# Kernel optimization log

Measured on AMD Instinct MI355X. Metric: run time of the kernel, lower is better.

## Reference

```python
import jax, jax.numpy as jnp
import numpy as np

DIM = 512; NHEAD = 8; DHEAD = 64; INNER = NHEAD * DHEAD
CTX = 1024; NOCT = int(np.ceil(np.log2(CTX))) + 1  # 11
B = 8; SEQ = 256; MEM = 768


def positional_encoding(ctx, num_oct):
    # matches Attention.positional_encoding on coords=arange(ctx).view(ctx,1),
    # start_octave = 1 - num_oct
    coords = jnp.arange(ctx, dtype=jnp.float32)[:, None, None]        # (ctx,1,1)
    octaves = jnp.arange(1 - num_oct, 1, dtype=jnp.float32)           # (num_oct,)
    mult = (2.0 ** octaves) * np.pi
    scaled = (coords * mult).reshape(ctx, num_oct)                    # (ctx, num_oct)
    return jnp.concatenate([jnp.sin(scaled), jnp.cos(scaled)], axis=-1)  # (ctx, 2*num_oct)


def get_shifts(mem, seq, ctx):
    coords = jnp.arange(mem + seq - 1, -1, -1) - (seq - 1)            # (mem+seq,)
    shifts = coords[None, :] + jnp.arange(seq)[:, None]               # (seq, mem+seq)
    oob = (shifts < 0) | (shifts > ctx - 1)
    bias = jnp.where(oob, -jnp.inf, 0.0).astype(jnp.float32)
    return jnp.clip(shifts, 0, ctx - 1), bias


def setup_inputs() -> dict:
    key = jax.random.key(0)
    ks = jax.random.split(key, 8)
    s = 0.02
    return {
        "x": jax.random.normal(ks[0], (B, SEQ, DIM), jnp.float32),
        "memory": jax.random.normal(ks[1], (B, MEM, DIM), jnp.float32),
        "W_qkv": jax.random.normal(ks[2], (DIM, 3 * INNER), jnp.float32) * s,
        "W_rel": jax.random.normal(ks[3], (2 * NOCT, INNER), jnp.float32) * s,
        "W_out": jax.random.normal(ks[4], (INNER, DIM), jnp.float32) * s,
        "b_out": jnp.zeros((DIM,), jnp.float32),
        "u_emb": jax.random.normal(ks[5], (DHEAD,), jnp.float32),
        "v_emb": jax.random.normal(ks[6], (DHEAD,), jnp.float32),
    }


def reference(x, memory, W_qkv, W_rel, W_out, b_out, u_emb, v_emb):
    b, seq, _ = x.shape
    mem = memory.shape[1]
    total = mem + seq
    scale = DHEAD ** -0.5

    shifts, bias = get_shifts(mem, seq, CTX)                          # (seq,total) each
    R = positional_encoding(CTX, NOCT)                                # (CTX, 2*NOCT)
    kr = (R @ W_rel)[shifts].reshape(seq, total, NHEAD, DHEAD)        # n m h d

    qkv = jnp.concatenate([memory, x], axis=1) @ W_qkv                # (b,total,3*INNER)
    q, k, v = jnp.split(qkv, 3, axis=-1)

    def heads(t):
        return t.reshape(b, total, NHEAD, DHEAD).transpose(0, 2, 1, 3)  # b h m d

    q = heads(q)[:, :, mem:]                                          # b h n d (queries only over x)
    k = heads(k)
    v = heads(v)

    term_a = jnp.einsum('bhnd,bhmd->bhnm', q, k)
    term_b = jnp.einsum('bhnd,nmhd->bhnm', q, kr)
    term_c = jnp.einsum('d,bhmd->bhm', u_emb, k)[:, :, None, :]        # broadcast over n
    term_d = jnp.einsum('d,nmhd->hnm', v_emb, kr)[None]                # broadcast over b

    dots = (term_a + term_b + term_c + term_d) * scale + bias          # banded -inf mask
    attn = jax.nn.softmax(dots, axis=-1)                               # dropout p=0 -> identity
    out = jnp.einsum('bhnm,bhmd->bnhd', attn, v).reshape(b, seq, INNER)
    return out @ W_out + b_out
```

## Files before the change

### kernel.cpp

```cpp
#include <hip/hip_runtime.h>
#include <hip/hip_bf16.h>
#include <math.h>

typedef unsigned short u16;
typedef unsigned int u32;
typedef __attribute__((ext_vector_type(8))) short short8;
typedef __attribute__((ext_vector_type(4))) float floatx4;

constexpr int kB     = 8;
constexpr int kSEQ   = 256;
constexpr int kMEM   = 768;
constexpr int kTOTAL = 1024;

__device__ __forceinline__ float bf2f(u16 u) {
  return __uint_as_float(((u32)u) << 16);
}
__device__ __forceinline__ u16 f2bf(float f) {
  __hip_bfloat16 h = __float2bfloat16(f);
  return *reinterpret_cast<u16*>(&h);
}
__device__ __forceinline__ void gload_lds16(const u16* g, u16* l) {
  __builtin_amdgcn_global_load_lds(
      (__attribute__((address_space(1))) const unsigned int*)g,
      (__attribute__((address_space(3))) unsigned int*)l, 16, 0, 0);
}

__global__ __launch_bounds__(256) void rrel_kernel(
    const float* __restrict__ W_rel, const float* __restrict__ v_emb,
    u16* __restrict__ Rrel_bf, float* __restrict__ vR)
{
  __shared__ float pe[22];
  __shared__ float prod[512];
  int s = blockIdx.x;
  int t = threadIdx.x;
  if (t < 22) {
    int o = (t < 11) ? t : (t - 11);
    float mult = ldexpf(3.14159265358979323846f, o - 10);
    float ang = (float)s * mult;
    pe[t] = (t < 11) ? sinf(ang) : cosf(ang);
  }
  __syncthreads();
#pragma unroll
  for (int c = 0; c < 2; c++) {
    int j = t + c * 256;
    float acc = 0.f;
#pragma unroll
    for (int o = 0; o < 22; ++o) acc += pe[o] * W_rel[o * 512 + j];
    Rrel_bf[(size_t)s * 512 + j] = f2bf(acc);
    prod[j] = acc * v_emb[j & 63];
  }
  __syncthreads();
  if (t < 8) {
    float a = 0.f;
#pragma unroll 8
    for (int d = 0; d < 64; d++) a += prod[t * 64 + d];
    vR[t * 1024 + s] = a * 0.125f;
  }
}

__device__ __forceinline__ void wtconv_body(
    const float* __restrict__ W, u16* __restrict__ Wt, int K, int N,
    int n0, int k0, int tid, float (*tile)[65])
{
  int r = tid >> 4, c4 = (tid & 15) * 4;
#pragma unroll
  for (int v = 0; v < 4; v++) {
    float4 w4 = *(const float4*)(W + (size_t)(k0 + v * 16 + r) * N + n0 + c4);
    tile[v * 16 + r][c4 + 0] = w4.x;
    tile[v * 16 + r][c4 + 1] = w4.y;
    tile[v * 16 + r][c4 + 2] = w4.z;
    tile[v * 16 + r][c4 + 3] = w4.w;
  }
  __syncthreads();
#pragma unroll
  for (int v = 0; v < 4; v++) {
    int rn = v * 16 + r;
    ushort4 o;
    o.x = f2bf(tile[c4 + 0][rn]);
    o.y = f2bf(tile[c4 + 1][rn]);
    o.z = f2bf(tile[c4 + 2][rn]);
    o.w = f2bf(tile[c4 + 3][rn]);
    *(ushort4*)(Wt + (size_t)(n0 + rn) * K + k0 + c4) = o;
  }
}

__global__ __launch_bounds__(256) void xw_kernel(
    const float* __restrict__ x, const float* __restrict__ memf,
    const float* __restrict__ W_qkv, const float* __restrict__ W_out,
    u16* __restrict__ Xb, u16* __restrict__ WqkvT, u16* __restrict__ WoutT)
{
  __shared__ float tile[64][65];
  int bid = blockIdx.x;
  int tid = threadIdx.x;
  if (bid < 2048) {
    int idx = bid * 256 + tid;
    int row = idx >> 6, c8 = idx & 63;
    int b = row >> 10, pos = row & 1023;
    const float* src = (pos < kMEM)
        ? memf + (size_t)(b * kMEM + pos) * 512
        : x    + (size_t)(b * kSEQ + pos - kMEM) * 512;
    const float4* s4 = (const float4*)(src + c8 * 8);
    float4 a = s4[0], bb = s4[1];
    u16 tmp[8] = {f2bf(a.x),  f2bf(a.y),  f2bf(a.z),  f2bf(a.w),
                  f2bf(bb.x), f2bf(bb.y), f2bf(bb.z), f2bf(bb.w)};
    *(uint4*)(Xb + (size_t)row * 512 + c8 * 8) = *(uint4*)tmp;
  } else if (bid < 2240) {
    int r = bid - 2048;
    wtconv_body(W_qkv, WqkvT, 512, 1536, (r % 24) * 64, (r / 24) * 64, tid, tile);
  } else {
    int r = bid - 2240;
    wtconv_body(W_out, WoutT, 512, 512, (r % 8) * 64, (r / 8) * 64, tid, tile);
  }
}

__global__ __launch_bounds__(256) void gemm_bf16(
    const u16* __restrict__ A, const u16* __restrict__ Bt,
    int lda, int ldb, int ksteps,
    u16* __restrict__ Cbf, float* __restrict__ Cf, int ldc,
    const float* __restrict__ colAdd, int mode)
{
  __shared__ u16 As[128 * 64];
  __shared__ u16 Bs[128 * 64];
  int tid = threadIdx.x;
  int id = blockIdx.y * gridDim.x + blockIdx.x;
  int gy = gridDim.y;
  int bm = (id % gy) * 128, bn = (id / gy) * 128;
  int ln = tid & 15, quad = (tid >> 4) & 3, w = tid >> 6;
  int moff = (w >> 1) * 64, noff = (w & 1) * 64;
  int l7 = ln & 7;
  floatx4 acc[4][4];
#pragma unroll
  for (int mi = 0; mi < 4; mi++)
#pragma unroll
    for (int ni = 0; ni < 4; ni++) acc[mi][ni] = (floatx4){0.f, 0.f, 0.f, 0.f};

  int srow[4], sgch[4];
#pragma unroll
  for (int v = 0; v < 4; v++) {
    int f = v * 256 + tid;
    srow[v] = f >> 3;
    sgch[v] = (f & 7) ^ ((f >> 3) & 7);
  }

  for (int ks = 0; ks < ksteps; ks++) {
    int k0 = ks * 64;
#pragma unroll
    for (int v = 0; v < 4; v++) {
      gload_lds16(A + (size_t)(bm + srow[v]) * lda + k0 + sgch[v] * 8,
                  &As[(v * 256 + tid) * 8]);
      gload_lds16(Bt + (size_t)(bn + srow[v]) * ldb + k0 + sgch[v] * 8,
                  &Bs[(v * 256 + tid) * 8]);
    }
    __syncthreads();
#pragma unroll
    for (int kb = 0; kb < 2; kb++) {
      short8 af[4], bfr[4];
#pragma unroll
      for (int mi = 0; mi < 4; mi++) {
        int row = moff + mi * 16 + ln;
        af[mi] = *(const short8*)&As[row * 64 + (((quad + 4 * kb) ^ l7) << 3)];
      }
#pragma unroll
      for (int ni = 0; ni < 4; ni++) {
        int row = noff + ni * 16 + ln;
        bfr[ni] = *(const short8*)&Bs[row * 64 + (((quad + 4 * kb) ^ l7) << 3)];
      }
#pragma unroll
      for (int mi = 0; mi < 4; mi++)
#pragma unroll
        for (int ni = 0; ni < 4; ni++)
          acc[mi][ni] = __builtin_amdgcn_mfma_f32_16x16x32_bf16(
              af[mi], bfr[ni], acc[mi][ni], 0, 0, 0);
    }
    __syncthreads();
  }

  int r0 = bm + moff + quad * 4;
#pragma unroll
  for (int ni = 0; ni < 4; ni++) {
    int col = bn + noff + ni * 16 + ln;
    float cv = (mode == 2) ? colAdd[col] : 0.f;
    float scale = (mode == 0 && col < 512) ? 0.125f : 1.f;
#pragma unroll
    for (int mi = 0; mi < 4; mi++) {
#pragma unroll
      for (int r = 0; r < 4; r++) {
        int row = r0 + mi * 16 + r;
        float val = acc[mi][ni][r];
        if (mode == 2) Cf[(size_t)row * ldc + col] = val + cv;
        else           Cbf[(size_t)row * ldc + col] = f2bf(val * scale);
      }
    }
  }
}

__global__ __launch_bounds__(256) void uk_kernel(
    const u16* __restrict__ qkv_bf, const float* __restrict__ u_emb,
    float* __restrict__ uk)
{
  int idx = blockIdx.x * 256 + threadIdx.x;
  int b = idx >> 13, h = (idx >> 10) & 7, m = idx & 1023;
  const u16* kp = qkv_bf + (size_t)(b * kTOTAL + m) * 1536 + 512 + h * 64;
  const float4* ue4 = (const float4*)u_emb;
  float acc = 0.f;
#pragma unroll
  for (int c = 0; c < 8; c++) {
    uint4 raw = *(const uint4*)(kp + c * 8);
    const u16* us = (const u16*)&raw;
    float4 ua = ue4[2 * c], ub = ue4[2 * c + 1];
    acc += bf2f(us[0]) * ua.x + bf2f(us[1]) * ua.y + bf2f(us[2]) * ua.z + bf2f(us[3]) * ua.w
         + bf2f(us[4]) * ub.x + bf2f(us[5]) * ub.y + bf2f(us[6]) * ub.z + bf2f(us[7]) * ub.w;
  }
  uk[idx] = acc * 0.125f;
}

__global__ __launch_bounds__(256) void attn_mfma(
    const u16* __restrict__ qkv_bf, const u16* __restrict__ Rrel_bf,
    const float* __restrict__ vR, const float* __restrict__ uk,
    u16* __restrict__ Opart, float* __restrict__ lbuf)
{
  constexpr int LD  = 72;
  constexpr int TLD = 84;
  __shared__ u16 Vt[2][64 * LD];
  __shared__ u16 Ps[64 * LD];
  __shared__ u16 Tl[4 * 16 * TLD];

  int nt = blockIdx.x >> 3, p = blockIdx.x & 7;
  int h = blockIdx.y, b = blockIdx.z;
  int n0 = nt * 64, bh = b * 8 + h;
  int tid = threadIdx.x;
  int w = tid >> 6, lane = tid & 63;
  int l15 = lane & 15, quad = lane >> 4, q8 = quad * 8;

  int sr0 = tid >> 3, sc8 = tid & 7;
  int sr1 = (256 + tid) >> 3;
  int vg0 = ((sr0 >> 3) ^ sc8) * 8 + (sr0 & 7);
  int vg1 = ((sr1 >> 3) ^ sc8) * 8 + (sr1 & 7);

  const u16* qrow = qkv_bf + (size_t)(b * kTOTAL + kMEM + n0 + 16 * w + l15) * 1536 + h * 64;
  short8 qf0 = *(const short8*)(qrow + q8);
  short8 qf1 = *(const short8*)(qrow + 32 + q8);

  const u16* kpart = qkv_bf + (size_t)(b * kTOTAL) * 1536 + 512 + h * 64;
  const float* ukrow = uk + (size_t)bh * 1024 + l15;
  const float* vRh = vR + h * 1024;
  u16* Tw = Tl + w * 16 * TLD;

  int ntiles = 13 + nt;
  int mtA = p, mtB = p + 8;
  bool hasB = (mtB < ntiles);
  bool lastB = (mtB == ntiles - 1);

  {
    const u16* va = kpart + (size_t)mtA * 64 * 1536 + 512;
    const u16* vb = kpart + (size_t)mtB * 64 * 1536 + 512;
    uint4 a0 = *(const uint4*)(va + (size_t)sr0 * 1536 + sc8 * 8);
    uint4 a1 = *(const uint4*)(va + (size_t)sr1 * 1536 + sc8 * 8);
    uint4 b0 = *(const uint4*)(vb + (size_t)sr0 * 1536 + sc8 * 8);
    uint4 b1 = *(const uint4*)(vb + (size_t)sr1 * 1536 + sc8 * 8);
    const u16* pa0v = (const u16*)&a0;
    const u16* pa1v = (const u16*)&a1;
    const u16* pb0v = (const u16*)&b0;
    const u16* pb1v = (const u16*)&b1;
#pragma unroll
    for (int i = 0; i < 8; i++) {
      Vt[0][(sc8 * 8 + i) * LD + vg0] = pa0v[i];
      Vt[0][(sc8 * 8 + i) * LD + vg1] = pa1v[i];
      Vt[1][(sc8 * 8 + i) * LD + vg0] = pb0v[i];
      Vt[1][(sc8 * 8 + i) * LD + vg1] = pb1v[i];
    }
  }
  __syncthreads();

  floatx4 o_acc[4];
  float l_i[4];
#pragma unroll
  for (int r = 0; r < 4; r++) l_i[r] = 0.f;
#pragma unroll
  for (int nd = 0; nd < 4; nd++) o_acc[nd] = (floatx4){0.f, 0.f, 0.f, 0.f};

  int s_base_w = kMEM + n0 + 16 * w;

  auto tile_body = [&](int mt, bool lastt, const u16* VtX) {
    int m0 = mt * 64;
    const u16* kbase = kpart + (size_t)m0 * 1536;
    int sb = s_base_w - m0;

    short8 kb0[4], kb1[4];
#pragma unroll
    for (int ni = 0; ni < 4; ni++) {
      const u16* kr = kbase + (size_t)(16 * ni + l15) * 1536;
      kb0[ni] = *(const short8*)(kr + q8);
      kb1[ni] = *(const short8*)(kr + 32 + q8);
    }
    short8 rb0[5], rb1[5];
    float vRc[5];
#pragma unroll
    for (int ct = 0; ct < 5; ct++) {
      int s = sb - 63 + 16 * ct + l15;
      s = min(max(s, 0), 1023);
      const u16* rr = Rrel_bf + (size_t)s * 512 + h * 64;
      rb0[ct] = *(const short8*)(rr + q8);
      rb1[ct] = *(const short8*)(rr + 32 + q8);
      vRc[ct] = vRh[s];
    }
    float ukc[4];
#pragma unroll
    for (int ni = 0; ni < 4; ni++) ukc[ni] = ukrow[m0 + ni * 16];

#pragma unroll
    for (int ct = 0; ct < 5; ct++) {
      floatx4 t = (floatx4){0.f, 0.f, 0.f, 0.f};
      t = __builtin_amdgcn_mfma_f32_16x16x32_bf16(qf0, rb0[ct], t, 0, 0, 0);
      t = __builtin_amdgcn_mfma_f32_16x16x32_bf16(qf1, rb1[ct], t, 0, 0, 0);
#pragma unroll
      for (int r = 0; r < 4; r++)
        Tw[(4 * quad + r) * TLD + 16 * ct + l15] = f2bf(t[r] + vRc[ct]);
    }

    floatx4 s_acc[4];
#pragma unroll
    for (int ni = 0; ni < 4; ni++) {
      floatx4 sa = (floatx4){0.f, 0.f, 0.f, 0.f};
      sa = __builtin_amdgcn_mfma_f32_16x16x32_bf16(qf0, kb0[ni], sa, 0, 0, 0);
      sa = __builtin_amdgcn_mfma_f32_16x16x32_bf16(qf1, kb1[ni], sa, 0, 0, 0);
      s_acc[ni] = sa;
    }

#pragma unroll
    for (int r = 0; r < 4; r++) {
      int il = 4 * quad + r;
      float ls = 0.f;
      float pv[4];
#pragma unroll
      for (int ni = 0; ni < 4; ni++) {
        float tsh = bf2f(Tw[il * TLD + 63 + il - 16 * ni - l15]);
        float val = s_acc[ni][r] + tsh + ukc[ni];
        if (lastt && (16 * ni + l15) > (16 * w + il)) val = -1e30f;
        float e = __expf(val);
        pv[ni] = e;
        ls += e;
      }
      l_i[r] += ls;
      int prow = 16 * w + il;
      int rr3p = prow >> 3;
      int base = prow * LD + (l15 & 7);
#pragma unroll
      for (int ni = 0; ni < 4; ni++)
        Ps[base + (((2 * ni + (l15 >> 3)) ^ rr3p) << 3)] = f2bf(pv[ni]);
    }

    int rowq = 16 * w + l15, rr3q = rowq >> 3;
    short8 pa0 = *(const short8*)&Ps[rowq * LD + ((quad ^ rr3q) << 3)];
    short8 pa1 = *(const short8*)&Ps[rowq * LD + (((quad + 4) ^ rr3q) << 3)];
#pragma unroll
    for (int nd = 0; nd < 4; nd++) {
      int rowv = 16 * nd + l15, rr3v = rowv >> 3;
      short8 vb0 = *(const short8*)&VtX[rowv * LD + ((quad ^ rr3v) << 3)];
      short8 vb1 = *(const short8*)&VtX[rowv * LD + (((quad + 4) ^ rr3v) << 3)];
      o_acc[nd] = __builtin_amdgcn_mfma_f32_16x16x32_bf16(pa0, vb0, o_acc[nd], 0, 0, 0);
      o_acc[nd] = __builtin_amdgcn_mfma_f32_16x16x32_bf16(pa1, vb1, o_acc[nd], 0, 0, 0);
    }
  };

  tile_body(mtA, false, Vt[0]);
  if (hasB) tile_body(mtB, lastB, Vt[1]);

  int pbase = (p * 64 + bh) * 256;
#pragma unroll
  for (int r = 0; r < 4; r++) {
    float l = l_i[r];
#pragma unroll
    for (int off = 1; off < 16; off <<= 1)
      l += __shfl_xor(l, off, 64);
    int n = n0 + 16 * w + 4 * quad + r;
    u16* orow = Opart + ((size_t)(pbase + n) << 6) + l15;
#pragma unroll
    for (int nd = 0; nd < 4; nd++)
      orow[16 * nd] = f2bf(o_acc[nd][r]);
    if (l15 == 0) lbuf[pbase + n] = l;
  }
}

__global__ __launch_bounds__(256) void attn_combine(
    const u16* __restrict__ Opart, const float* __restrict__ lbuf,
    u16* __restrict__ aout_bf)
{
  int idx = blockIdx.x * 256 + threadIdx.x;
  int bh = idx >> 12, n = (idx >> 4) & 255, d4 = idx & 15;
  int rowi = bh * 256 + n;
  float den = 0.f;
  float num[4] = {0.f, 0.f, 0.f, 0.f};
#pragma unroll
  for (int p = 0; p < 8; p++) {
    den += lbuf[(p << 14) + rowi];
    uint2 raw = *(const uint2*)(Opart + (((size_t)(p << 14) + rowi) << 6) + d4 * 4);
    const u16* us = (const u16*)&raw;
#pragma unroll
    for (int j = 0; j < 4; j++) num[j] += bf2f(us[j]);
  }
  float inv = 1.f / den;
  int b = bh >> 3, h = bh & 7;
  ushort4 o;
  o.x = f2bf(num[0] * inv);
  o.y = f2bf(num[1] * inv);
  o.z = f2bf(num[2] * inv);
  o.w = f2bf(num[3] * inv);
  *(ushort4*)(aout_bf + (size_t)(b * kSEQ + n) * 512 + h * 64 + d4 * 4) = o;
}

extern "C" void kernel_launch(void* const* d_in, const int* in_sizes, int n_in,
                              void* d_out, int out_size, void* d_ws, size_t ws_size,
                              hipStream_t stream) {
  (void)in_sizes; (void)n_in; (void)out_size; (void)ws_size;
  const float* x      = (const float*)d_in[0];
  const float* memory = (const float*)d_in[1];
  const float* W_qkv  = (const float*)d_in[2];
  const float* W_rel  = (const float*)d_in[3];
  const float* W_out  = (const float*)d_in[4];
  const float* b_out  = (const float*)d_in[5];
  const float* u_emb  = (const float*)d_in[6];
  const float* v_emb  = (const float*)d_in[7];
  float* out = (float*)d_out;

  char* ws = (char*)d_ws;
  u16*   qkv_bf  = (u16*)ws;                         ws += (size_t)12582912 * 2;
  u16*   Xcat_bf = (u16*)ws;                         ws += (size_t)4194304 * 2;
  u16*   aout_bf = (u16*)ws;                         ws += (size_t)1048576 * 2;
  u16*   Opart   = (u16*)ws;                         ws += (size_t)8388608 * 2;
  float* lbuf    = (float*)ws;                       ws += (size_t)131072 * 4;
  u16*   WqkvT   = (u16*)ws;                         ws += (size_t)786432 * 2;
  u16*   WoutT   = (u16*)ws;                         ws += (size_t)262144 * 2;
  u16*   Rrel_bf = (u16*)ws;                         ws += (size_t)524288 * 2;
  float* vR      = (float*)ws;                       ws += (size_t)8192 * 4;
  float* uk      = (float*)ws;                       ws += (size_t)65536 * 4;

  rrel_kernel<<<1024, 256, 0, stream>>>(W_rel, v_emb, Rrel_bf, vR);
  xw_kernel<<<2304, 256, 0, stream>>>(x, memory, W_qkv, W_out, Xcat_bf, WqkvT, WoutT);

  gemm_bf16<<<dim3(12, 64), 256, 0, stream>>>(
      Xcat_bf, WqkvT, 512, 512, 8, qkv_bf, nullptr, 1536, nullptr, 0);

  uk_kernel<<<256, 256, 0, stream>>>(qkv_bf, u_emb, uk);

  attn_mfma<<<dim3(32, 8, 8), 256, 0, stream>>>(qkv_bf, Rrel_bf, vR, uk, Opart, lbuf);
  attn_combine<<<1024, 256, 0, stream>>>(Opart, lbuf, aout_bf);

  gemm_bf16<<<dim3(4, 16), 256, 0, stream>>>(
      aout_bf, WoutT, 512, 512, 8, nullptr, out, 512, b_out, 2);
}
```

Baseline: 170.3 us.

## Merge prep kernels, fold u·k into attention MFMA, retile output GEMM

Merges the relative-embedding kernel into the input/weight conversion kernel, which cuts one launch. Removes the separate uk kernel by computing the u·k bias inside the attention kernel with two extra MFMAs per key tile, using a bf16 copy of u_emb pre-scaled by 0.125. Replaces the 128x128 output GEMM (64 blocks) with a 64x64-tile variant (256 blocks) to fill more CUs. The trade-off is extra MFMA work inside attention and bf16 rounding of u_emb.

```diff
diff --git a/kernel.cpp b/kernel.cpp
--- a/kernel.cpp
+++ b/kernel.cpp
@@ -23,39 +23,6 @@
   __builtin_amdgcn_global_load_lds(
       (__attribute__((address_space(1))) const unsigned int*)g,
       (__attribute__((address_space(3))) unsigned int*)l, 16, 0, 0);
-}
-
-__global__ __launch_bounds__(256) void rrel_kernel(
-    const float* __restrict__ W_rel, const float* __restrict__ v_emb,
-    u16* __restrict__ Rrel_bf, float* __restrict__ vR)
-{
-  __shared__ float pe[22];
-  __shared__ float prod[512];
-  int s = blockIdx.x;
-  int t = threadIdx.x;
-  if (t < 22) {
-    int o = (t < 11) ? t : (t - 11);
-    float mult = ldexpf(3.14159265358979323846f, o - 10);
-    float ang = (float)s * mult;
-    pe[t] = (t < 11) ? sinf(ang) : cosf(ang);
-  }
-  __syncthreads();
-#pragma unroll
-  for (int c = 0; c < 2; c++) {
-    int j = t + c * 256;
-    float acc = 0.f;
-#pragma unroll
-    for (int o = 0; o < 22; ++o) acc += pe[o] * W_rel[o * 512 + j];
-    Rrel_bf[(size_t)s * 512 + j] = f2bf(acc);
-    prod[j] = acc * v_emb[j & 63];
-  }
-  __syncthreads();
-  if (t < 8) {
-    float a = 0.f;
-#pragma unroll 8
-    for (int d = 0; d < 64; d++) a += prod[t * 64 + d];
-    vR[t * 1024 + s] = a * 0.125f;
-  }
 }
 
 __device__ __forceinline__ void wtconv_body(
@@ -84,16 +51,45 @@
   }
 }
 
-__global__ __launch_bounds__(256) void xw_kernel(
+__global__ __launch_bounds__(256) void prep_kernel(
     const float* __restrict__ x, const float* __restrict__ memf,
     const float* __restrict__ W_qkv, const float* __restrict__ W_out,
-    u16* __restrict__ Xb, u16* __restrict__ WqkvT, u16* __restrict__ WoutT)
+    const float* __restrict__ W_rel, const float* __restrict__ v_emb,
+    u16* __restrict__ Xb, u16* __restrict__ WqkvT, u16* __restrict__ WoutT,
+    u16* __restrict__ Rrel_bf, float* __restrict__ vR)
 {
   __shared__ float tile[64][65];
+  __shared__ float pe[22];
+  __shared__ float prod[512];
   int bid = blockIdx.x;
-  int tid = threadIdx.x;
-  if (bid < 2048) {
-    int idx = bid * 256 + tid;
+  int t = threadIdx.x;
+  if (bid < 1024) {
+    int s = bid;
+    if (t < 22) {
+      int o = (t < 11) ? t : (t - 11);
+      float mult = ldexpf(3.14159265358979323846f, o - 10);
+      float ang = (float)s * mult;
+      pe[t] = (t < 11) ? sinf(ang) : cosf(ang);
+    }
+    __syncthreads();
+#pragma unroll
+    for (int c = 0; c < 2; c++) {
+      int j = t + c * 256;
+      float acc = 0.f;
+#pragma unroll
+      for (int o = 0; o < 22; ++o) acc += pe[o] * W_rel[o * 512 + j];
+      Rrel_bf[(size_t)s * 512 + j] = f2bf(acc);
+      prod[j] = acc * v_emb[j & 63];
+    }
+    __syncthreads();
+    if (t < 8) {
+      float a = 0.f;
+#pragma unroll 8
+      for (int d = 0; d < 64; d++) a += prod[t * 64 + d];
+      vR[t * 1024 + s] = a * 0.125f;
+    }
+  } else if (bid < 3072) {
+    int idx = (bid - 1024) * 256 + t;
     int row = idx >> 6, c8 = idx & 63;
     int b = row >> 10, pos = row & 1023;
     const float* src = (pos < kMEM)
@@ -104,20 +100,19 @@
     u16 tmp[8] = {f2bf(a.x),  f2bf(a.y),  f2bf(a.z),  f2bf(a.w),
                   f2bf(bb.x), f2bf(bb.y), f2bf(bb.z), f2bf(bb.w)};
     *(uint4*)(Xb + (size_t)row * 512 + c8 * 8) = *(uint4*)tmp;
-  } else if (bid < 2240) {
-    int r = bid - 2048;
-    wtconv_body(W_qkv, WqkvT, 512, 1536, (r % 24) * 64, (r / 24) * 64, tid, tile);
+  } else if (bid < 3264) {
+    int r = bid - 3072;
+    wtconv_body(W_qkv, WqkvT, 512, 1536, (r % 24) * 64, (r / 24) * 64, t, tile);
   } else {
-    int r = bid - 2240;
-    wtconv_body(W_out, WoutT, 512, 512, (r % 8) * 64, (r / 8) * 64, tid, tile);
+    int r = bid - 3264;
+    wtconv_body(W_out, WoutT, 512, 512, (r % 8) * 64, (r / 8) * 64, t, tile);
   }
 }
 
 __global__ __launch_bounds__(256) void gemm_bf16(
     const u16* __restrict__ A, const u16* __restrict__ Bt,
     int lda, int ldb, int ksteps,
-    u16* __restrict__ Cbf, float* __restrict__ Cf, int ldc,
-    const float* __restrict__ colAdd, int mode)
+    u16* __restrict__ Cbf, int ldc, int qscale)
 {
   __shared__ u16 As[128 * 64];
   __shared__ u16 Bs[128 * 64];
@@ -179,44 +174,98 @@
 #pragma unroll
   for (int ni = 0; ni < 4; ni++) {
     int col = bn + noff + ni * 16 + ln;
-    float cv = (mode == 2) ? colAdd[col] : 0.f;
-    float scale = (mode == 0 && col < 512) ? 0.125f : 1.f;
+    float scale = (qscale && col < 512) ? 0.125f : 1.f;
 #pragma unroll
     for (int mi = 0; mi < 4; mi++) {
 #pragma unroll
       for (int r = 0; r < 4; r++) {
         int row = r0 + mi * 16 + r;
-        float val = acc[mi][ni][r];
-        if (mode == 2) Cf[(size_t)row * ldc + col] = val + cv;
-        else           Cbf[(size_t)row * ldc + col] = f2bf(val * scale);
-      }
-    }
-  }
-}
-
-__global__ __launch_bounds__(256) void uk_kernel(
-    const u16* __restrict__ qkv_bf, const float* __restrict__ u_emb,
-    float* __restrict__ uk)
+        Cbf[(size_t)row * ldc + col] = f2bf(acc[mi][ni][r] * scale);
+      }
+    }
+  }
+}
+
+__global__ __launch_bounds__(256) void gemm_bf16_64(
+    const u16* __restrict__ A, const u16* __restrict__ Bt,
+    int lda, int ldb, int ksteps,
+    float* __restrict__ Cf, int ldc, const float* __restrict__ bias)
 {
-  int idx = blockIdx.x * 256 + threadIdx.x;
-  int b = idx >> 13, h = (idx >> 10) & 7, m = idx & 1023;
-  const u16* kp = qkv_bf + (size_t)(b * kTOTAL + m) * 1536 + 512 + h * 64;
-  const float4* ue4 = (const float4*)u_emb;
-  float acc = 0.f;
-#pragma unroll
-  for (int c = 0; c < 8; c++) {
-    uint4 raw = *(const uint4*)(kp + c * 8);
-    const u16* us = (const u16*)&raw;
-    float4 ua = ue4[2 * c], ub = ue4[2 * c + 1];
-    acc += bf2f(us[0]) * ua.x + bf2f(us[1]) * ua.y + bf2f(us[2]) * ua.z + bf2f(us[3]) * ua.w
-         + bf2f(us[4]) * ub.x + bf2f(us[5]) * ub.y + bf2f(us[6]) * ub.z + bf2f(us[7]) * ub.w;
-  }
-  uk[idx] = acc * 0.125f;
+  __shared__ u16 As[64 * 64];
+  __shared__ u16 Bs[64 * 64];
+  int tid = threadIdx.x;
+  int id = blockIdx.y * gridDim.x + blockIdx.x;
+  int gy = gridDim.y;
+  int bm = (id % gy) * 64, bn = (id / gy) * 64;
+  int ln = tid & 15, quad = (tid >> 4) & 3, w = tid >> 6;
+  int moff = (w >> 1) * 32, noff = (w & 1) * 32;
+  int l7 = ln & 7;
+  floatx4 acc[2][2];
+#pragma unroll
+  for (int mi = 0; mi < 2; mi++)
+#pragma unroll
+    for (int ni = 0; ni < 2; ni++) acc[mi][ni] = (floatx4){0.f, 0.f, 0.f, 0.f};
+
+  int srow[2], sgch[2];
+#pragma unroll
+  for (int v = 0; v < 2; v++) {
+    int f = v * 256 + tid;
+    srow[v] = f >> 3;
+    sgch[v] = (f & 7) ^ ((f >> 3) & 7);
+  }
+
+  for (int ks = 0; ks < ksteps; ks++) {
+    int k0 = ks * 64;
+#pragma unroll
+    for (int v = 0; v < 2; v++) {
+      gload_lds16(A + (size_t)(bm + srow[v]) * lda + k0 + sgch[v] * 8,
+                  &As[(v * 256 + tid) * 8]);
+      gload_lds16(Bt + (size_t)(bn + srow[v]) * ldb + k0 + sgch[v] * 8,
+                  &Bs[(v * 256 + tid) * 8]);
+    }
+    __syncthreads();
+#pragma unroll
+    for (int kb = 0; kb < 2; kb++) {
+      short8 af[2], bfr[2];
+#pragma unroll
+      for (int mi = 0; mi < 2; mi++) {
+        int row = moff + mi * 16 + ln;
+        af[mi] = *(const short8*)&As[row * 64 + (((quad + 4 * kb) ^ l7) << 3)];
+      }
+#pragma unroll
+      for (int ni = 0; ni < 2; ni++) {
+        int row = noff + ni * 16 + ln;
+        bfr[ni] = *(const short8*)&Bs[row * 64 + (((quad + 4 * kb) ^ l7) << 3)];
+      }
+#pragma unroll
+      for (int mi = 0; mi < 2; mi++)
+#pragma unroll
+        for (int ni = 0; ni < 2; ni++)
+          acc[mi][ni] = __builtin_amdgcn_mfma_f32_16x16x32_bf16(
+              af[mi], bfr[ni], acc[mi][ni], 0, 0, 0);
+    }
+    __syncthreads();
+  }
+
+  int r0 = bm + moff + quad * 4;
+#pragma unroll
+  for (int ni = 0; ni < 2; ni++) {
+    int col = bn + noff + ni * 16 + ln;
+    float cv = bias[col];
+#pragma unroll
+    for (int mi = 0; mi < 2; mi++) {
+#pragma unroll
+      for (int r = 0; r < 4; r++) {
+        int row = r0 + mi * 16 + r;
+        Cf[(size_t)row * ldc + col] = acc[mi][ni][r] + cv;
+      }
+    }
+  }
 }
 
 __global__ __launch_bounds__(256) void attn_mfma(
     const u16* __restrict__ qkv_bf, const u16* __restrict__ Rrel_bf,
-    const float* __restrict__ vR, const float* __restrict__ uk,
+    const float* __restrict__ vR, const float* __restrict__ u_emb,
     u16* __restrict__ Opart, float* __restrict__ lbuf)
 {
   constexpr int LD  = 72;
@@ -241,8 +290,19 @@
   short8 qf0 = *(const short8*)(qrow + q8);
   short8 qf1 = *(const short8*)(qrow + 32 + q8);
 
+  short8 uf0, uf1;
+  {
+    u16 t0[8], t1[8];
+#pragma unroll
+    for (int j = 0; j < 8; j++) {
+      t0[j] = f2bf(0.125f * u_emb[q8 + j]);
+      t1[j] = f2bf(0.125f * u_emb[32 + q8 + j]);
+    }
+    uf0 = *(short8*)t0;
+    uf1 = *(short8*)t1;
+  }
+
   const u16* kpart = qkv_bf + (size_t)(b * kTOTAL) * 1536 + 512 + h * 64;
-  const float* ukrow = uk + (size_t)bh * 1024 + l15;
   const float* vRh = vR + h * 1024;
   u16* Tw = Tl + w * 16 * TLD;
 
@@ -304,9 +364,15 @@
       rb1[ct] = *(const short8*)(rr + 32 + q8);
       vRc[ct] = vRh[s];
     }
-    float ukc[4];
-#pragma unroll
-    for (int ni = 0; ni < 4; ni++) ukc[ni] = ukrow[m0 + ni * 16];
+
+    floatx4 uku[4];
+#pragma unroll
+    for (int ni = 0; ni < 4; ni++) {
+      floatx4 ua = (floatx4){0.f, 0.f, 0.f, 0.f};
+      ua = __builtin_amdgcn_mfma_f32_16x16x32_bf16(uf0, kb0[ni], ua, 0, 0, 0);
+      ua = __builtin_amdgcn_mfma_f32_16x16x32_bf16(uf1, kb1[ni], ua, 0, 0, 0);
+      uku[ni] = ua;
+    }
 
 #pragma unroll
     for (int ct = 0; ct < 5; ct++) {
@@ -335,7 +401,7 @@
 #pragma unroll
       for (int ni = 0; ni < 4; ni++) {
         float tsh = bf2f(Tw[il * TLD + 63 + il - 16 * ni - l15]);
-        float val = s_acc[ni][r] + tsh + ukc[ni];
+        float val = s_acc[ni][r] + tsh + uku[ni][r];
         if (lastt && (16 * ni + l15) > (16 * w + il)) val = -1e30f;
         float e = __expf(val);
         pv[ni] = e;
@@ -433,19 +499,18 @@
   u16*   WoutT   = (u16*)ws;                         ws += (size_t)262144 * 2;
   u16*   Rrel_bf = (u16*)ws;                         ws += (size_t)524288 * 2;
   float* vR      = (float*)ws;                       ws += (size_t)8192 * 4;
-  float* uk      = (float*)ws;                       ws += (size_t)65536 * 4;
-
-  rrel_kernel<<<1024, 256, 0, stream>>>(W_rel, v_emb, Rrel_bf, vR);
-  xw_kernel<<<2304, 256, 0, stream>>>(x, memory, W_qkv, W_out, Xcat_bf, WqkvT, WoutT);
+
+  prep_kernel<<<3328, 256, 0, stream>>>(
+      x, memory, W_qkv, W_out, W_rel, v_emb, Xcat_bf, WqkvT, WoutT, Rrel_bf, vR);
 
   gemm_bf16<<<dim3(12, 64), 256, 0, stream>>>(
-      Xcat_bf, WqkvT, 512, 512, 8, qkv_bf, nullptr, 1536, nullptr, 0);
-
-  uk_kernel<<<256, 256, 0, stream>>>(qkv_bf, u_emb, uk);
-
-  attn_mfma<<<dim3(32, 8, 8), 256, 0, stream>>>(qkv_bf, Rrel_bf, vR, uk, Opart, lbuf);
+      Xcat_bf, WqkvT, 512, 512, 8, qkv_bf, 1536, 1);
+
+  attn_mfma<<<dim3(32, 8, 8), 256, 0, stream>>>(
+      qkv_bf, Rrel_bf, vR, u_emb, Opart, lbuf);
+
   attn_combine<<<1024, 256, 0, stream>>>(Opart, lbuf, aout_bf);
 
-  gemm_bf16<<<dim3(4, 16), 256, 0, stream>>>(
-      aout_bf, WoutT, 512, 512, 8, nullptr, out, 512, b_out, 2);
-}
+  gemm_bf16_64<<<dim3(8, 32), 256, 0, stream>>>(
+      aout_bf, WoutT, 512, 512, 8, out, 512, b_out);
+}
```

After: 158.7 us. -6.8%, faster.
